# Performance work log

Hardware: AMD Instinct MI355X
Metric: run time of the kernel (lower is better)

The kernel has to match this reference:

```python
import jax, jax.numpy as jnp
import numpy as np
from jax import lax

# ---- static config (matches init_kwargs) ----
BATCH, SEQ, D_MODEL = 2, 512, 1024
D_STATE, EXPAND, HEADDIM, D_CONV = 64, 2, 64, 4
VNUM, HORIZON = 3, 20
D_INNER = EXPAND * D_MODEL            # 2048
NHEADS = D_INNER // HEADDIM           # 32
CONV_DIM = D_INNER + 2 * D_STATE      # x, B, C go through the depthwise conv
D_IN_PROJ = 2 * D_INNER + 2 * D_STATE + NHEADS  # z | xBC | dt
RMS_EPS = 1e-5


def setup_inputs() -> dict:
    key = jax.random.key(0)
    ks = jax.random.split(key, 10)
    s = 0.02
    return {
        "embed_data": jax.random.normal(ks[0], (BATCH, SEQ, D_MODEL), jnp.float32),
        "in_proj_w": (jax.random.normal(ks[1], (D_IN_PROJ, D_MODEL), jnp.float32) * s),
        "conv_w": (jax.random.normal(ks[2], (CONV_DIM, D_CONV), jnp.float32) * s),
        "conv_b": jnp.zeros((CONV_DIM,), jnp.float32),
        # dt_bias = softplus^{-1}(dt_init) with dt_init ~ U(1e-3, 0.1), as in Mamba2
        "dt_bias": jnp.log(jnp.expm1(jax.random.uniform(ks[3], (NHEADS,), jnp.float32, 1e-3, 0.1))),
        # A = -exp(A_log), A_init ~ U(1, 16)
        "A_log": jnp.log(jax.random.uniform(ks[4], (NHEADS,), jnp.float32, 1.0, 16.0)),
        "D": jnp.ones((NHEADS,), jnp.float32),
        "norm_w": jnp.ones((D_INNER,), jnp.float32),
        "out_proj_w": (jax.random.normal(ks[5], (D_MODEL, D_INNER), jnp.float32) * s),
        "dec_cur_w": (jax.random.normal(ks[6], (VNUM, D_MODEL), jnp.float32) * s),
        "dec_cur_b": jnp.zeros((VNUM,), jnp.float32),
        "dec_fut_w": (jax.random.normal(ks[7], (HORIZON * VNUM, D_MODEL), jnp.float32) * s),
        "dec_fut_b": jnp.zeros((HORIZON * VNUM,), jnp.float32),
    }


def _mamba2(embed_data, in_proj_w, conv_w, conv_b, dt_bias, A_log, D, norm_w, out_proj_w):
    b, s, _ = embed_data.shape
    zxbcdt = jnp.einsum('bsd,ed->bse', embed_data, in_proj_w)  # [B,S,D_IN_PROJ]
    z = zxbcdt[..., :D_INNER]
    xBC = zxbcdt[..., D_INNER:D_INNER + CONV_DIM]
    dt = zxbcdt[..., D_INNER + CONV_DIM:]                      # [B,S,H]

    # causal depthwise conv1d (kernel=4) + silu
    xpad = jnp.pad(xBC, ((0, 0), (D_CONV - 1, 0), (0, 0)))
    xBC = sum(conv_w[:, k] * xpad[:, k:k + s, :] for k in range(D_CONV)) + conv_b
    xBC = jax.nn.silu(xBC)

    x = xBC[..., :D_INNER].reshape(b, s, NHEADS, HEADDIM)       # [B,S,H,P]
    Bm = xBC[..., D_INNER:D_INNER + D_STATE]                    # [B,S,N]
    Cm = xBC[..., D_INNER + D_STATE:]                           # [B,S,N]

    dt = jax.nn.softplus(dt + dt_bias)                          # [B,S,H]
    A = -jnp.exp(A_log)                                         # [H]

    # selective state-space scan: h_t = exp(dt*A) h_{t-1} + dt * x_t B_t^T
    def step(h, inp):
        x_t, dt_t, b_t, c_t = inp                               # [B,H,P],[B,H],[B,N],[B,N]
        dA = jnp.exp(dt_t * A)                                  # [B,H]
        h = h * dA[..., None, None] + (dt_t[..., None] * x_t)[..., None] * b_t[:, None, None, :]
        y = jnp.einsum('bhpn,bn->bhp', h, c_t)
        return h, y

    h0 = jnp.zeros((b, NHEADS, HEADDIM, D_STATE), embed_data.dtype)
    xs = (x.transpose(1, 0, 2, 3), dt.transpose(1, 0, 2),
          Bm.transpose(1, 0, 2), Cm.transpose(1, 0, 2))
    _, ys = lax.scan(step, h0, xs)                              # [S,B,H,P]
    y = ys.transpose(1, 0, 2, 3) + D[None, None, :, None] * x   # skip term D*x
    y = y.reshape(b, s, D_INNER)

    # gated RMSNorm: rmsnorm(y * silu(z)) * w
    y = y * jax.nn.silu(z)
    y = y * lax.rsqrt(jnp.mean(y * y, axis=-1, keepdims=True) + RMS_EPS) * norm_w
    return jnp.einsum('bsi,di->bsd', y, out_proj_w)             # [B,S,D_MODEL]


def reference(embed_data, in_proj_w, conv_w, conv_b, dt_bias, A_log, D, norm_w,
              out_proj_w, dec_cur_w, dec_cur_b, dec_fut_w, dec_fut_b):
    h = _mamba2(embed_data, in_proj_w, conv_w, conv_b, dt_bias, A_log, D, norm_w, out_proj_w)
    pred_current = jnp.einsum('bsd,vd->bsv', h, dec_cur_w) + dec_cur_b         # [B,S,V]
    pred_future = (h[:, -1] @ dec_fut_w.T + dec_fut_b).reshape(h.shape[0], HORIZON, VNUM)
    return (pred_current, pred_future)
```

## Files before the change

### kernel.cpp

```cpp
#include <hip/hip_runtime.h>
#include <hip/hip_bf16.h>

#define BATCH   2
#define SEQ     512
#define DMODEL  1024
#define DSTATE  64
#define HEADDIM 64
#define DCONV   4
#define VNUM    3
#define HORIZON 20
#define DINNER  2048
#define NHEADS  32
#define CONVDIM 2176
#define DINPROJ 4256
#define NPAD1   4352
#define BS      (BATCH*SEQ)
#define RMS_EPS 1e-5f
#define CHUNK   64
#define NCHUNK  (SEQ/CHUNK)
#define NDEC    (VNUM + HORIZON*VNUM)
#define WC_DS   32
#define LDB     72

typedef __attribute__((ext_vector_type(8))) short bf16x8;
typedef __attribute__((ext_vector_type(4))) float f32x4;

__device__ __forceinline__ unsigned short f2b(float x) {
    union { float f; unsigned u; } v; v.f = x;
    return (unsigned short)((v.u + 0x7fffu + ((v.u >> 16) & 1u)) >> 16);
}

__device__ __forceinline__ float silu(float x) { return x / (1.f + expf(-x)); }

__device__ __forceinline__ void async16(const void* g, const void* l) {
    __builtin_amdgcn_global_load_lds(
        (const __attribute__((address_space(1))) unsigned int*)g,
        (__attribute__((address_space(3))) unsigned int*)l, 16, 0, 0);
}

template<int BM, int BN, int FM, int FN, int KD>
__global__ __launch_bounds__(256) void gemm_bf16(const short* __restrict__ A,
                                                 const short* __restrict__ B,
                                                 float* __restrict__ C, int N) {
    constexpr int WM = FM * 16, WN = FN * 16;
    static_assert(BM == 2 * WM && BN == 2 * WN, "2x2 waves");
    __shared__ __align__(16) short At[BM * 32];
    __shared__ __align__(16) short Bt[BN * 32];
    const int t    = threadIdx.x;
    const int lane = t & 63;
    const int w    = t >> 6;
    const int wm   = (w >> 1) * WM, wn = (w & 1) * WN;
    const int row0 = blockIdx.y * BM, col0 = blockIdx.x * BN;
    const int fr   = lane & 15;
    const int kq   = lane >> 4;
    const int lr   = t >> 2;
    const int lc   = (t & 3) * 8;

    const short* Ag = A + (size_t)(row0 + lr) * KD + lc;
    const short* Bg = B + (size_t)(col0 + lr) * KD + lc;

    f32x4 acc[FM][FN];
#pragma unroll
    for (int i = 0; i < FM; ++i)
#pragma unroll
        for (int j = 0; j < FN; ++j)
#pragma unroll
            for (int r = 0; r < 4; ++r) acc[i][j][r] = 0.f;

    for (int k0 = 0; k0 < KD; k0 += 32) {
        __syncthreads();
#pragma unroll
        for (int i = 0; i < BM / 64; ++i)
            async16(Ag + (size_t)i * 64 * KD + k0, (const char*)At + i * 4096 + t * 16);
#pragma unroll
        for (int i = 0; i < BN / 64; ++i)
            async16(Bg + (size_t)i * 64 * KD + k0, (const char*)Bt + i * 4096 + t * 16);
        __syncthreads();

        bf16x8 af[FM], bv[FN];
#pragma unroll
        for (int i = 0; i < FM; ++i)
            af[i] = *(const bf16x8*)&At[(wm + i * 16 + fr) * 32 + kq * 8];
#pragma unroll
        for (int j = 0; j < FN; ++j)
            bv[j] = *(const bf16x8*)&Bt[(wn + j * 16 + fr) * 32 + kq * 8];
#pragma unroll
        for (int i = 0; i < FM; ++i)
#pragma unroll
            for (int j = 0; j < FN; ++j)
                acc[i][j] = __builtin_amdgcn_mfma_f32_16x16x32_bf16(
                    af[i], bv[j], acc[i][j], 0, 0, 0);
    }

    const int orow = lane >> 4;
#pragma unroll
    for (int i = 0; i < FM; ++i)
#pragma unroll
        for (int j = 0; j < FN; ++j) {
            const int col = col0 + wn + j * 16 + fr;
            if (col < N) {
#pragma unroll
                for (int r = 0; r < 4; ++r) {
                    const int row = row0 + wm + i * 16 + orow * 4 + r;
                    C[(size_t)row * N + col] = acc[i][j][r];
                }
            }
        }
}

#define EMB4     (BS * DMODEL / 4)
#define IPW4     (NPAD1 * DMODEL / 4)
#define CASTBLKS ((EMB4 + IPW4) / 256)
__global__ __launch_bounds__(256) void prep_kernel(
        const float* __restrict__ embed, const float* __restrict__ ipw,
        short* __restrict__ embB, short* __restrict__ ipwB,
        const float* __restrict__ op, const float* __restrict__ cwv,
        const float* __restrict__ fwv, float* __restrict__ P) {
    __shared__ float lw[32][64];
    if (blockIdx.x < CASTBLKS) {
        const int i = blockIdx.x * 256 + threadIdx.x;
        if (i < EMB4) {
            float4 v = *(const float4*)(embed + (size_t)i * 4);
            *(short4*)(embB + (size_t)i * 4) =
                make_short4((short)f2b(v.x), (short)f2b(v.y),
                            (short)f2b(v.z), (short)f2b(v.w));
        } else {
            const int j = i - EMB4;
            const size_t e0 = (size_t)j * 4;
            const int row = (int)(e0 / DMODEL);
            short4 o;
            if (row < DINPROJ) {
                float4 v = *(const float4*)(ipw + e0);
                o = make_short4((short)f2b(v.x), (short)f2b(v.y),
                                (short)f2b(v.z), (short)f2b(v.w));
            } else {
                o = make_short4(0, 0, 0, 0);
            }
            *(short4*)(ipwB + e0) = o;
        }
        return;
    }
    const int blk   = blockIdx.x - CASTBLKS;
    const int itile = blk & 7;
    const int ds    = blk >> 3;
    const int i     = itile * 256 + threadIdx.x;
    const int d0    = ds * 32;

#pragma unroll
    for (int k = 0; k < 8; ++k) {
        const int e = threadIdx.x * 8 + k;
        const int d = e >> 6, v = e & 63;
        float val = 0.f;
        if (v < VNUM)      val = cwv[(size_t)v * DMODEL + d0 + d];
        else if (v < NDEC) val = fwv[(size_t)(v - VNUM) * DMODEL + d0 + d];
        lw[d][v] = val;
    }

    float opc[32];
#pragma unroll
    for (int d = 0; d < 32; ++d) opc[d] = op[(size_t)(d0 + d) * DINNER + i];
    __syncthreads();

    f32x4 acc[16];
#pragma unroll
    for (int q = 0; q < 16; ++q)
#pragma unroll
        for (int r = 0; r < 4; ++r) acc[q][r] = 0.f;

#pragma unroll
    for (int d = 0; d < 32; ++d) {
        const float o = opc[d];
#pragma unroll
        for (int q = 0; q < 16; ++q) {
            float4 wv = *(const float4*)&lw[d][q * 4];
            acc[q][0] += o * wv.x; acc[q][1] += o * wv.y;
            acc[q][2] += o * wv.z; acc[q][3] += o * wv.w;
        }
    }

    float* Pp = P + (size_t)ds * 64 * DINNER + i;
#pragma unroll
    for (int q = 0; q < 16; ++q)
#pragma unroll
        for (int r = 0; r < 4; ++r)
            Pp[(size_t)(q * 4 + r) * DINNER] = acc[q][r];
}

#define CONVBLKS (BS * CONVDIM / 4 / 256)
__global__ __launch_bounds__(256) void conv_kernel(
        const float* __restrict__ zxbcdt, const float* __restrict__ cw,
        const float* __restrict__ cb, float* __restrict__ xbc) {
    const int item = blockIdx.x * 256 + threadIdx.x;
    const int c4 = item % (CONVDIM / 4);
    const int rs = item / (CONVDIM / 4);
    const int s  = rs % SEQ;
    const int c  = c4 * 4;
    const float* src = zxbcdt + (size_t)rs * DINPROJ + DINNER + c;
    float4 x0 = (s >= 3) ? *(const float4*)(src - 3 * DINPROJ) : make_float4(0,0,0,0);
    float4 x1 = (s >= 2) ? *(const float4*)(src - 2 * DINPROJ) : make_float4(0,0,0,0);
    float4 x2 = (s >= 1) ? *(const float4*)(src - 1 * DINPROJ) : make_float4(0,0,0,0);
    float4 x3 = *(const float4*)(src);
    float4 bias = *(const float4*)(cb + c);
    float4 r;
    { float4 w = *(const float4*)(cw + (size_t)(c+0)*4);
      r.x = bias.x + w.x*x0.x + w.y*x1.x + w.z*x2.x + w.w*x3.x; }
    { float4 w = *(const float4*)(cw + (size_t)(c+1)*4);
      r.y = bias.y + w.x*x0.y + w.y*x1.y + w.z*x2.y + w.w*x3.y; }
    { float4 w = *(const float4*)(cw + (size_t)(c+2)*4);
      r.z = bias.z + w.x*x0.z + w.y*x1.z + w.z*x2.z + w.w*x3.z; }
    { float4 w = *(const float4*)(cw + (size_t)(c+3)*4);
      r.w = bias.w + w.x*x0.w + w.y*x1.w + w.z*x2.w + w.w*x3.w; }
    r.x = silu(r.x); r.y = silu(r.y); r.z = silu(r.z); r.w = silu(r.w);
    *(float4*)(xbc + (size_t)rs * CONVDIM + c) = r;
}

__global__ __launch_bounds__(256) void chunk_intra_kernel(
        const float* __restrict__ zx, const float* __restrict__ xbc,
        const float* __restrict__ dt_bias, const float* __restrict__ A_log,
        const float* __restrict__ Dv, float* __restrict__ yraw,
        float* __restrict__ Sc, float* __restrict__ dexp) {
    const int blk = blockIdx.x;
    const int c  = blk & 7;
    const int bh = blk >> 3;
    const int h  = bh & 31;
    const int b  = bh >> 5;
    const int rs0 = b * SEQ + c * CHUNK;

    __shared__ __align__(16) short sB [64 * LDB];
    __shared__ __align__(16) short sCt[64 * LDB];
    __shared__ __align__(16) short sBn[64 * LDB];
    __shared__ __align__(16) short sUt[64 * LDB];
    __shared__ __align__(16) short sUe[64 * LDB];
    __shared__ __align__(16) short sM [64 * LDB];
    __shared__ float sl[64], se[64], sdt[64];

    const int tid  = threadIdx.x;
    const int lane = tid & 63;
    const int w    = tid >> 6;
    const int fr   = lane & 15;
    const int kq   = lane >> 4;
    const int wm   = w * 16;
    const float A  = -expf(A_log[h]);

    {
        const int row = tid >> 2;
        const int cq  = tid & 3;
        const float* xrow = xbc + (size_t)(rs0 + row) * CONVDIM + DINNER;
#pragma unroll
        for (int i = 0; i < 4; ++i) {
            const int n = cq * 16 + i * 4;
            float4 bv = *(const float4*)(xrow + n);
            float4 cv = *(const float4*)(xrow + DSTATE + n);
            short4 bs = make_short4((short)f2b(bv.x), (short)f2b(bv.y),
                                    (short)f2b(bv.z), (short)f2b(bv.w));
            short4 cs = make_short4((short)f2b(cv.x), (short)f2b(cv.y),
                                    (short)f2b(cv.z), (short)f2b(cv.w));
            *(short4*)&sB [row * LDB + n] = bs;
            *(short4*)&sCt[row * LDB + n] = cs;
            sBn[(n+0) * LDB + row] = bs.x;
            sBn[(n+1) * LDB + row] = bs.y;
            sBn[(n+2) * LDB + row] = bs.z;
            sBn[(n+3) * LDB + row] = bs.w;
        }
    }

    if (tid < 64) {
        const float raw = zx[(size_t)(rs0 + tid) * DINPROJ + DINNER + CONVDIM + h]
                          + dt_bias[h];
        const float dtv = fmaxf(raw, 0.f) + log1pf(expf(-fabsf(raw)));
        sdt[tid] = dtv;
        float v = dtv * A;
#pragma unroll
        for (int off = 1; off < 64; off <<= 1) {
            float o = __shfl_up(v, off, 64);
            if (tid >= off) v += o;
        }
        sl[tid] = v;
        const float ltot = __shfl(v, 63, 64);
        se[tid] = expf(ltot - v);
        dexp[(size_t)blk * 64 + tid] = expf(v);
    }
    __syncthreads();

    f32x4 accM[4];
#pragma unroll
    for (int j = 0; j < 4; ++j)
#pragma unroll
        for (int r = 0; r < 4; ++r) accM[j][r] = 0.f;
#pragma unroll
    for (int k0 = 0; k0 < 64; k0 += 32) {
        bf16x8 af = *(const bf16x8*)&sCt[(wm + fr) * LDB + kq * 8 + k0];
#pragma unroll
        for (int j = 0; j < 4; ++j) {
            bf16x8 bv = *(const bf16x8*)&sB[(j * 16 + fr) * LDB + kq * 8 + k0];
            accM[j] = __builtin_amdgcn_mfma_f32_16x16x32_bf16(af, bv, accM[j], 0, 0, 0);
        }
    }
    {
        const int t0 = wm + kq * 4;
        const float lt0 = sl[t0+0], lt1 = sl[t0+1], lt2 = sl[t0+2], lt3 = sl[t0+3];
#pragma unroll
        for (int j = 0; j < 4; ++j) {
            const int s = j * 16 + fr;
            const float ls = sl[s];
            sM[(t0+0)*LDB + s] = (short)f2b((s <= t0+0) ? expf(lt0-ls)*accM[j][0] : 0.f);
            sM[(t0+1)*LDB + s] = (short)f2b((s <= t0+1) ? expf(lt1-ls)*accM[j][1] : 0.f);
            sM[(t0+2)*LDB + s] = (short)f2b((s <= t0+2) ? expf(lt2-ls)*accM[j][2] : 0.f);
            sM[(t0+3)*LDB + s] = (short)f2b((s <= t0+3) ? expf(lt3-ls)*accM[j][3] : 0.f);
        }
    }

    {
        const int row = tid >> 2;
        const int cq  = tid & 3;
        const float dtv = sdt[row];
        const float sev = se[row];
        const float* xr = xbc + (size_t)(rs0 + row) * CONVDIM + h * HEADDIM;
#pragma unroll
        for (int i = 0; i < 4; ++i) {
            const int p = cq * 16 + i * 4;
            float4 xv = *(const float4*)(xr + p);
            const float u0 = dtv * xv.x, u1 = dtv * xv.y;
            const float u2 = dtv * xv.z, u3 = dtv * xv.w;
            sUt[(p+0)*LDB + row] = (short)f2b(u0);
            sUt[(p+1)*LDB + row] = (short)f2b(u1);
            sUt[(p+2)*LDB + row] = (short)f2b(u2);
            sUt[(p+3)*LDB + row] = (short)f2b(u3);
            sUe[(p+0)*LDB + row] = (short)f2b(u0 * sev);
            sUe[(p+1)*LDB + row] = (short)f2b(u1 * sev);
            sUe[(p+2)*LDB + row] = (short)f2b(u2 * sev);
            sUe[(p+3)*LDB + row] = (short)f2b(u3 * sev);
        }
    }
    __syncthreads();

    f32x4 accY[4];
#pragma unroll
    for (int j = 0; j < 4; ++j)
#pragma unroll
        for (int r = 0; r < 4; ++r) accY[j][r] = 0.f;
#pragma unroll
    for (int k0 = 0; k0 < 64; k0 += 32) {
        bf16x8 af = *(const bf16x8*)&sM[(wm + fr) * LDB + kq * 8 + k0];
#pragma unroll
        for (int j = 0; j < 4; ++j) {
            bf16x8 bv = *(const bf16x8*)&sUt[(j * 16 + fr) * LDB + kq * 8 + k0];
            accY[j] = __builtin_amdgcn_mfma_f32_16x16x32_bf16(af, bv, accY[j], 0, 0, 0);
        }
    }
    f32x4 accS[4];
#pragma unroll
    for (int j = 0; j < 4; ++j)
#pragma unroll
        for (int r = 0; r < 4; ++r) accS[j][r] = 0.f;
#pragma unroll
    for (int k0 = 0; k0 < 64; k0 += 32) {
        bf16x8 af = *(const bf16x8*)&sUe[(wm + fr) * LDB + kq * 8 + k0];
#pragma unroll
        for (int j = 0; j < 4; ++j) {
            bf16x8 bv = *(const bf16x8*)&sBn[(j * 16 + fr) * LDB + kq * 8 + k0];
            accS[j] = __builtin_amdgcn_mfma_f32_16x16x32_bf16(af, bv, accS[j], 0, 0, 0);
        }
    }

    {
        const float Dh = Dv[h];
        const int t0 = wm + kq * 4;
#pragma unroll
        for (int r = 0; r < 4; ++r) {
            const int t = t0 + r;
            const float* xr = xbc + (size_t)(rs0 + t) * CONVDIM + h * HEADDIM;
            float* yr = yraw + (size_t)(rs0 + t) * DINNER + h * HEADDIM;
#pragma unroll
            for (int j = 0; j < 4; ++j) {
                const int p = j * 16 + fr;
                yr[p] = accY[j][r] + Dh * xr[p];
            }
        }
    }
    {
        float* scp = Sc + (size_t)blk * (HEADDIM * DSTATE);
        const int p0 = wm + kq * 4;
#pragma unroll
        for (int r = 0; r < 4; ++r)
#pragma unroll
            for (int j = 0; j < 4; ++j)
                scp[(size_t)(p0 + r) * DSTATE + j * 16 + fr] = accS[j][r];
    }
}

__global__ __launch_bounds__(256) void comb_reduce_kernel(
        const float* __restrict__ Sc, const float* __restrict__ dexp,
        float* __restrict__ h0ws, const float* __restrict__ P,
        float* __restrict__ W) {
    if (blockIdx.x < 256) {
        const int bh = blockIdx.x >> 2;
        const int e  = (blockIdx.x & 3) * 1024 + threadIdx.x * 4;
        float4 h = make_float4(0.f, 0.f, 0.f, 0.f);
        for (int c = 0; c < NCHUNK; ++c) {
            const size_t base = (size_t)(bh * NCHUNK + c) * (HEADDIM * DSTATE);
            const float ac = dexp[(size_t)(bh * NCHUNK + c) * 64 + 63];
            *(float4*)&h0ws[base + e] = h;
            float4 s = *(const float4*)&Sc[base + e];
            h.x = ac * h.x + s.x; h.y = ac * h.y + s.y;
            h.z = ac * h.z + s.z; h.w = ac * h.w + s.w;
        }
    } else {
        const int idx = (blockIdx.x - 256) * 256 + threadIdx.x;
        float s = 0.f;
#pragma unroll
        for (int ds = 0; ds < WC_DS; ++ds) s += P[(size_t)ds * 64 * DINNER + idx];
        W[idx] = s;
    }
}

__global__ __launch_bounds__(256) void chunk_state_out_kernel(
        const float* __restrict__ xbc, const float* __restrict__ h0ws,
        const float* __restrict__ dexp, float* __restrict__ yraw) {
    const int blk = blockIdx.x;
    const int c  = blk & 7;
    if (c == 0) return;
    const int bh = blk >> 3;
    const int h  = bh & 31;
    const int b  = bh >> 5;
    const int rs0 = b * SEQ + c * CHUNK;

    __shared__ __align__(16) short sCt[64 * LDB];
    __shared__ __align__(16) short sH [64 * LDB];
    __shared__ float sdex[64];

    const int tid  = threadIdx.x;
    const int lane = tid & 63;
    const int w    = tid >> 6;
    const int fr   = lane & 15;
    const int kq   = lane >> 4;
    const int wm   = w * 16;
    {
        const int row = tid >> 2;
        const int cq  = tid & 3;
        const float* xrow = xbc + (size_t)(rs0 + row) * CONVDIM + DINNER + DSTATE;
        const float* hrow = h0ws + (size_t)blk * (HEADDIM * DSTATE)
                            + (size_t)row * DSTATE;
#pragma unroll
        for (int i = 0; i < 4; ++i) {
            const int n = cq * 16 + i * 4;
            float4 cv = *(const float4*)(xrow + n);
            float4 hv = *(const float4*)(hrow + n);
            *(short4*)&sCt[row * LDB + n] =
                make_short4((short)f2b(cv.x), (short)f2b(cv.y),
                            (short)f2b(cv.z), (short)f2b(cv.w));
            *(short4*)&sH[row * LDB + n] =
                make_short4((short)f2b(hv.x), (short)f2b(hv.y),
                            (short)f2b(hv.z), (short)f2b(hv.w));
        }
    }
    if (tid < 64) sdex[tid] = dexp[(size_t)blk * 64 + tid];
    __syncthreads();

    f32x4 acc[4];
#pragma unroll
    for (int j = 0; j < 4; ++j)
#pragma unroll
        for (int r = 0; r < 4; ++r) acc[j][r] = 0.f;
#pragma unroll
    for (int k0 = 0; k0 < 64; k0 += 32) {
        bf16x8 af = *(const bf16x8*)&sCt[(wm + fr) * LDB + kq * 8 + k0];
#pragma unroll
        for (int j = 0; j < 4; ++j) {
            bf16x8 bv = *(const bf16x8*)&sH[(j * 16 + fr) * LDB + kq * 8 + k0];
            acc[j] = __builtin_amdgcn_mfma_f32_16x16x32_bf16(af, bv, acc[j], 0, 0, 0);
        }
    }
    const int t0 = wm + kq * 4;
#pragma unroll
    for (int r = 0; r < 4; ++r) {
        const int t = t0 + r;
        const float d = sdex[t];
        float* yr = yraw + (size_t)(rs0 + t) * DINNER + h * HEADDIM;
#pragma unroll
        for (int j = 0; j < 4; ++j) {
            const int p = j * 16 + fr;
            yr[p] += d * acc[j][r];
        }
    }
}

__global__ __launch_bounds__(256) void gate_norm_pred_kernel(
        const float* __restrict__ zxbcdt, const float* __restrict__ y,
        const float* __restrict__ nw, const float* __restrict__ W,
        const float* __restrict__ cur_b, float* __restrict__ out,
        float* __restrict__ ylast) {
    const int rs = blockIdx.x;
    const int t  = threadIdx.x;
    const float* z  = zxbcdt + (size_t)rs * DINPROJ;
    const float* yr = y + (size_t)rs * DINNER;

    float vals[8];
    float ss = 0.f;
#pragma unroll
    for (int i = 0; i < 8; ++i) {
        const int c = t + i * 256;
        const float zv = z[c];
        const float v  = yr[c] * (zv / (1.f + expf(-zv)));
        vals[i] = v;
        ss += v * v;
    }
#pragma unroll
    for (int off = 32; off > 0; off >>= 1) ss += __shfl_down(ss, off, 64);
    __shared__ float red[4];
    if ((t & 63) == 0) red[t >> 6] = ss;
    __syncthreads();
    const float tot   = red[0] + red[1] + red[2] + red[3];
    const float scale = rsqrtf(tot / (float)DINNER + RMS_EPS);

    const bool is_last = ((rs & (SEQ - 1)) == SEQ - 1);
    float p0 = 0.f, p1 = 0.f, p2 = 0.f;
#pragma unroll
    for (int i = 0; i < 8; ++i) {
        const int c = t + i * 256;
        const float vn = vals[i] * scale * nw[c];
        vals[i] = vn;
        p0 += vn * W[c];
        p1 += vn * W[DINNER + c];
        p2 += vn * W[2 * DINNER + c];
    }
    if (is_last) {
        float* yl = ylast + (size_t)(rs >> 9) * DINNER;
#pragma unroll
        for (int i = 0; i < 8; ++i) yl[t + i * 256] = vals[i];
    }
#pragma unroll
    for (int off = 32; off > 0; off >>= 1) {
        p0 += __shfl_down(p0, off, 64);
        p1 += __shfl_down(p1, off, 64);
        p2 += __shfl_down(p2, off, 64);
    }
    __shared__ float r3[4][3];
    if ((t & 63) == 0) { r3[t >> 6][0] = p0; r3[t >> 6][1] = p1; r3[t >> 6][2] = p2; }
    __syncthreads();
    if (t < VNUM) {
        const float s = r3[0][t] + r3[1][t] + r3[2][t] + r3[3][t];
        out[(size_t)rs * VNUM + t] = s + cur_b[t];
    }
}

__global__ __launch_bounds__(256) void pred_fut_kernel(
        const float* __restrict__ ylast, const float* __restrict__ W,
        const float* __restrict__ bvec, float* __restrict__ out) {
    const int blk = blockIdx.x;
    const int b = blk / (HORIZON * VNUM);
    const int j = blk % (HORIZON * VNUM);
    const float* yl = ylast + (size_t)b * DINNER;
    const float* wr = W + (size_t)(VNUM + j) * DINNER;
    float pv = 0.f;
    for (int i = threadIdx.x; i < DINNER; i += 256) pv += yl[i] * wr[i];
#pragma unroll
    for (int off = 32; off > 0; off >>= 1) pv += __shfl_down(pv, off, 64);
    __shared__ float red[4];
    if ((threadIdx.x & 63) == 0) red[threadIdx.x >> 6] = pv;
    __syncthreads();
    if (threadIdx.x == 0)
        out[b * (HORIZON * VNUM) + j] = red[0] + red[1] + red[2] + red[3] + bvec[j];
}

extern "C" void kernel_launch(void* const* d_in, const int* in_sizes, int n_in,
                              void* d_out, int out_size, void* d_ws, size_t ws_size,
                              hipStream_t stream) {
    const float* embed      = (const float*)d_in[0];
    const float* in_proj_w  = (const float*)d_in[1];
    const float* conv_w     = (const float*)d_in[2];
    const float* conv_b     = (const float*)d_in[3];
    const float* dt_bias    = (const float*)d_in[4];
    const float* A_log      = (const float*)d_in[5];
    const float* Dv         = (const float*)d_in[6];
    const float* norm_w     = (const float*)d_in[7];
    const float* out_proj_w = (const float*)d_in[8];
    const float* dec_cur_w  = (const float*)d_in[9];
    const float* dec_cur_b  = (const float*)d_in[10];
    const float* dec_fut_w  = (const float*)d_in[11];
    const float* dec_fut_b  = (const float*)d_in[12];

    float* ws     = (float*)d_ws;
    float* zxbcdt = ws;
    float* xbc    = zxbcdt + (size_t)BS * DINPROJ;
    float* yraw   = xbc    + (size_t)BS * CONVDIM;
    float* Sc     = yraw   + (size_t)BS * DINNER;
    float* h0ws   = Sc     + (size_t)BATCH*NHEADS*NCHUNK*HEADDIM*DSTATE;
    float* dexp   = h0ws   + (size_t)BATCH*NHEADS*NCHUNK*HEADDIM*DSTATE;
    float* Wp     = dexp   + (size_t)BATCH*NHEADS*NCHUNK*64;
    float* W      = Wp     + (size_t)WC_DS * 64 * DINNER;
    float* ylast  = W      + (size_t)64 * DINNER;
    short* embB   = (short*)(ylast + (size_t)BATCH * DINNER);
    short* ipwB   = embB + (size_t)BS * DMODEL;

    float* out = (float*)d_out;

    prep_kernel<<<CASTBLKS + 8 * WC_DS, 256, 0, stream>>>(
        embed, in_proj_w, embB, ipwB, out_proj_w, dec_cur_w, dec_fut_w, Wp);

    gemm_bf16<128, 64, 4, 2, DMODEL>
        <<<dim3(NPAD1 / 64, BS / 128), 256, 0, stream>>>(embB, ipwB, zxbcdt, DINPROJ);

    conv_kernel<<<CONVBLKS, 256, 0, stream>>>(zxbcdt, conv_w, conv_b, xbc);

    chunk_intra_kernel<<<BATCH * NHEADS * NCHUNK, 256, 0, stream>>>(
        zxbcdt, xbc, dt_bias, A_log, Dv, yraw, Sc, dexp);

    comb_reduce_kernel<<<256 + 64 * DINNER / 256, 256, 0, stream>>>(
        Sc, dexp, h0ws, Wp, W);

    chunk_state_out_kernel<<<BATCH * NHEADS * NCHUNK, 256, 0, stream>>>(
        xbc, h0ws, dexp, yraw);

    gate_norm_pred_kernel<<<BS, 256, 0, stream>>>(zxbcdt, yraw, norm_w, W,
                                                  dec_cur_b, out, ylast);

    pred_fut_kernel<<<BATCH * HORIZON * VNUM, 256, 0, stream>>>(ylast, W, dec_fut_b,
                                                                out + BS * VNUM);
}
```

Measured before the change: 176.8 us.

## Fold chunk-state scan into chunk_intra via last-block atomic counter

```diff
diff --git a/kernel.cpp b/kernel.cpp
--- a/kernel.cpp
+++ b/kernel.cpp
@@ -115,8 +115,11 @@
         const float* __restrict__ embed, const float* __restrict__ ipw,
         short* __restrict__ embB, short* __restrict__ ipwB,
         const float* __restrict__ op, const float* __restrict__ cwv,
-        const float* __restrict__ fwv, float* __restrict__ P) {
+        const float* __restrict__ fwv, float* __restrict__ P,
+        int* __restrict__ cnt) {
     __shared__ float lw[32][64];
+    if (blockIdx.x == 0 && threadIdx.x < BATCH * NHEADS)
+        cnt[threadIdx.x] = 0;
     if (blockIdx.x < CASTBLKS) {
         const int i = blockIdx.x * 256 + threadIdx.x;
         if (i < EMB4) {
@@ -187,9 +190,19 @@
 }
 
 #define CONVBLKS (BS * CONVDIM / 4 / 256)
-__global__ __launch_bounds__(256) void conv_kernel(
+#define WREDBLKS (64 * DINNER / 256)
+__global__ __launch_bounds__(256) void conv_wred_kernel(
         const float* __restrict__ zxbcdt, const float* __restrict__ cw,
-        const float* __restrict__ cb, float* __restrict__ xbc) {
+        const float* __restrict__ cb, float* __restrict__ xbc,
+        const float* __restrict__ P, float* __restrict__ W) {
+    if (blockIdx.x >= CONVBLKS) {
+        const int idx = (blockIdx.x - CONVBLKS) * 256 + threadIdx.x;
+        float s = 0.f;
+#pragma unroll
+        for (int ds = 0; ds < WC_DS; ++ds) s += P[(size_t)ds * 64 * DINNER + idx];
+        W[idx] = s;
+        return;
+    }
     const int item = blockIdx.x * 256 + threadIdx.x;
     const int c4 = item % (CONVDIM / 4);
     const int rs = item / (CONVDIM / 4);
@@ -218,7 +231,7 @@
         const float* __restrict__ zx, const float* __restrict__ xbc,
         const float* __restrict__ dt_bias, const float* __restrict__ A_log,
         const float* __restrict__ Dv, float* __restrict__ yraw,
-        float* __restrict__ Sc, float* __restrict__ dexp) {
+        float* Sc, float* dexp, int* cnt) {
     const int blk = blockIdx.x;
     const int c  = blk & 7;
     const int bh = blk >> 3;
@@ -233,6 +246,7 @@
     __shared__ __align__(16) short sUe[64 * LDB];
     __shared__ __align__(16) short sM [64 * LDB];
     __shared__ float sl[64], se[64], sdt[64];
+    __shared__ int slast;
 
     const int tid  = threadIdx.x;
     const int lane = tid & 63;
@@ -387,35 +401,40 @@
             for (int j = 0; j < 4; ++j)
                 scp[(size_t)(p0 + r) * DSTATE + j * 16 + fr] = accS[j][r];
     }
-}
-
-__global__ __launch_bounds__(256) void comb_reduce_kernel(
-        const float* __restrict__ Sc, const float* __restrict__ dexp,
-        float* __restrict__ h0ws, const float* __restrict__ P,
-        float* __restrict__ W) {
-    if (blockIdx.x < 256) {
-        const int bh = blockIdx.x >> 2;
-        const int e  = (blockIdx.x & 3) * 1024 + threadIdx.x * 4;
-        float4 h = make_float4(0.f, 0.f, 0.f, 0.f);
-        for (int c = 0; c < NCHUNK; ++c) {
-            const size_t base = (size_t)(bh * NCHUNK + c) * (HEADDIM * DSTATE);
-            const float ac = dexp[(size_t)(bh * NCHUNK + c) * 64 + 63];
-            *(float4*)&h0ws[base + e] = h;
-            float4 s = *(const float4*)&Sc[base + e];
-            h.x = ac * h.x + s.x; h.y = ac * h.y + s.y;
-            h.z = ac * h.z + s.z; h.w = ac * h.w + s.w;
-        }
-    } else {
-        const int idx = (blockIdx.x - 256) * 256 + threadIdx.x;
-        float s = 0.f;
-#pragma unroll
-        for (int ds = 0; ds < WC_DS; ++ds) s += P[(size_t)ds * 64 * DINNER + idx];
-        W[idx] = s;
+
+    __threadfence();
+    __syncthreads();
+    if (tid == 0) {
+        int old = __hip_atomic_fetch_add(&cnt[bh], 1, __ATOMIC_ACQ_REL,
+                                         __HIP_MEMORY_SCOPE_AGENT);
+        slast = (old == NCHUNK - 1) ? 1 : 0;
+    }
+    __syncthreads();
+    if (slast) {
+        __threadfence();
+        const int e = tid * 4;
+        float4 hq[4];
+#pragma unroll
+        for (int k = 0; k < 4; ++k) hq[k] = make_float4(0.f, 0.f, 0.f, 0.f);
+        const size_t tb = (size_t)(bh * NCHUNK) * (HEADDIM * DSTATE);
+        for (int cc = 0; cc < NCHUNK; ++cc) {
+            float* scp2 = Sc + tb + (size_t)cc * (HEADDIM * DSTATE);
+            const float ac = dexp[(size_t)(bh * NCHUNK + cc) * 64 + 63];
+#pragma unroll
+            for (int k = 0; k < 4; ++k) {
+                float4 s = *(const float4*)&scp2[e + k * 1024];
+                *(float4*)&scp2[e + k * 1024] = hq[k];
+                hq[k].x = ac * hq[k].x + s.x;
+                hq[k].y = ac * hq[k].y + s.y;
+                hq[k].z = ac * hq[k].z + s.z;
+                hq[k].w = ac * hq[k].w + s.w;
+            }
+        }
     }
 }
 
 __global__ __launch_bounds__(256) void chunk_state_out_kernel(
-        const float* __restrict__ xbc, const float* __restrict__ h0ws,
+        const float* __restrict__ xbc, const float* __restrict__ Sc,
         const float* __restrict__ dexp, float* __restrict__ yraw) {
     const int blk = blockIdx.x;
     const int c  = blk & 7;
@@ -439,7 +458,7 @@
         const int row = tid >> 2;
         const int cq  = tid & 3;
         const float* xrow = xbc + (size_t)(rs0 + row) * CONVDIM + DINNER + DSTATE;
-        const float* hrow = h0ws + (size_t)blk * (HEADDIM * DSTATE)
+        const float* hrow = Sc + (size_t)blk * (HEADDIM * DSTATE)
                             + (size_t)row * DSTATE;
 #pragma unroll
         for (int i = 0; i < 4; ++i) {
@@ -585,32 +604,30 @@
     float* xbc    = zxbcdt + (size_t)BS * DINPROJ;
     float* yraw   = xbc    + (size_t)BS * CONVDIM;
     float* Sc     = yraw   + (size_t)BS * DINNER;
-    float* h0ws   = Sc     + (size_t)BATCH*NHEADS*NCHUNK*HEADDIM*DSTATE;
-    float* dexp   = h0ws   + (size_t)BATCH*NHEADS*NCHUNK*HEADDIM*DSTATE;
+    float* dexp   = Sc     + (size_t)BATCH*NHEADS*NCHUNK*HEADDIM*DSTATE;
     float* Wp     = dexp   + (size_t)BATCH*NHEADS*NCHUNK*64;
     float* W      = Wp     + (size_t)WC_DS * 64 * DINNER;
     float* ylast  = W      + (size_t)64 * DINNER;
     short* embB   = (short*)(ylast + (size_t)BATCH * DINNER);
     short* ipwB   = embB + (size_t)BS * DMODEL;
+    int*   cnt    = (int*)(ipwB + (size_t)NPAD1 * DMODEL);
 
     float* out = (float*)d_out;
 
     prep_kernel<<<CASTBLKS + 8 * WC_DS, 256, 0, stream>>>(
-        embed, in_proj_w, embB, ipwB, out_proj_w, dec_cur_w, dec_fut_w, Wp);
+        embed, in_proj_w, embB, ipwB, out_proj_w, dec_cur_w, dec_fut_w, Wp, cnt);
 
     gemm_bf16<128, 64, 4, 2, DMODEL>
         <<<dim3(NPAD1 / 64, BS / 128), 256, 0, stream>>>(embB, ipwB, zxbcdt, DINPROJ);
 
-    conv_kernel<<<CONVBLKS, 256, 0, stream>>>(zxbcdt, conv_w, conv_b, xbc);
+    conv_wred_kernel<<<CONVBLKS + WREDBLKS, 256, 0, stream>>>(
+        zxbcdt, conv_w, conv_b, xbc, Wp, W);
 
     chunk_intra_kernel<<<BATCH * NHEADS * NCHUNK, 256, 0, stream>>>(
-        zxbcdt, xbc, dt_bias, A_log, Dv, yraw, Sc, dexp);
-
-    comb_reduce_kernel<<<256 + 64 * DINNER / 256, 256, 0, stream>>>(
-        Sc, dexp, h0ws, Wp, W);
+        zxbcdt, xbc, dt_bias, A_log, Dv, yraw, Sc, dexp, cnt);
 
     chunk_state_out_kernel<<<BATCH * NHEADS * NCHUNK, 256, 0, stream>>>(
-        xbc, h0ws, dexp, yraw);
+        xbc, Sc, dexp, yraw);
 
     gate_norm_pred_kernel<<<BS, 256, 0, stream>>>(zxbcdt, yraw, norm_w, W,
                                                   dec_cur_b, out, ylast);
```

Measured after the change: 277.5 us. 56.9% more time.
